# Kernel optimization log

Hardware: AMD Instinct MI355X
Metric: run time of the kernel (lower is better)

## Reference

```python
import jax, jax.numpy as jnp
import numpy as np

NB, NC = 100000, 10000   # buildings, communities
EB, EC = 400000, 80000   # edges
BD, CD = 64, 32          # feature dims


def _glorot(key, shape):
    fan_in = shape[-2] if len(shape) > 1 else shape[0]
    return jax.random.normal(key, shape, jnp.float32) * (1.0 / np.sqrt(fan_in))


def setup_inputs() -> dict:
    key = jax.random.key(0)
    ks = iter(jax.random.split(key, 40))
    inp = {}
    inp['building_features'] = jax.random.normal(next(ks), (NB, BD), jnp.float32)
    inp['community_features'] = jax.random.normal(next(ks), (NC, CD), jnp.float32)
    inp['building_edge_index'] = jax.random.randint(next(ks), (2, EB), 0, NB, jnp.int32)
    inp['community_edge_index'] = jax.random.randint(next(ks), (2, EC), 0, NC, jnp.int32)
    inp['building_to_comm_mapping'] = jax.random.randint(next(ks), (NB,), 0, NC, jnp.int32)
    inp['c1_wl'] = _glorot(next(ks), (CD, 512)); inp['c1_wr'] = _glorot(next(ks), (CD, 512))
    inp['c1_att'] = _glorot(next(ks), (8, 64)); inp['c1_b'] = jnp.zeros((512,), jnp.float32)
    inp['c2_wl'] = _glorot(next(ks), (512, 128)); inp['c2_wr'] = _glorot(next(ks), (512, 128))
    inp['c2_att'] = _glorot(next(ks), (4, 32)); inp['c2_b'] = jnp.zeros((128,), jnp.float32)
    # feature attention: 8 heads of MLP (64+128)->128->2
    inp['fa_w1'] = _glorot(next(ks), (8, BD + 128, 128)); inp['fa_b1'] = jnp.zeros((8, 128), jnp.float32)
    inp['fa_w2'] = _glorot(next(ks), (8, 128, 2)); inp['fa_b2'] = jnp.zeros((8, 2), jnp.float32)
    inp['b1_wl'] = _glorot(next(ks), (BD + 128, 512)); inp['b1_wr'] = _glorot(next(ks), (BD + 128, 512))
    inp['b1_att'] = _glorot(next(ks), (8, 64)); inp['b1_b'] = jnp.zeros((512,), jnp.float32)
    inp['b2_wl'] = _glorot(next(ks), (512, 128)); inp['b2_wr'] = _glorot(next(ks), (512, 128))
    inp['b2_att'] = _glorot(next(ks), (4, 32)); inp['b2_b'] = jnp.zeros((128,), jnp.float32)
    inp['b3_wl'] = _glorot(next(ks), (128, 2)); inp['b3_wr'] = _glorot(next(ks), (128, 2))
    inp['b3_att'] = _glorot(next(ks), (1, 2)); inp['b3_b'] = jnp.zeros((2,), jnp.float32)
    return inp


def gatv2(x, src, dst, wl, wr, att, b, heads, out_dim, concat=True):
    """PyG GATv2Conv (eval mode, self-loops already appended to src/dst)."""
    n = x.shape[0]
    xl = (x @ wl).reshape(n, heads, out_dim)  # source transform
    xr = (x @ wr).reshape(n, heads, out_dim)  # target transform
    e = jax.nn.leaky_relu(xl[src] + xr[dst], 0.2)          # [E,H,D]
    logits = jnp.einsum('ehd,hd->eh', e, att)              # [E,H]
    m = jax.ops.segment_max(logits, dst, num_segments=n)   # stable softmax per target
    p = jnp.exp(logits - m[dst])
    denom = jax.ops.segment_sum(p, dst, num_segments=n)
    alpha = p / denom[dst]
    agg = jax.ops.segment_sum(alpha[:, :, None] * xl[src], dst, num_segments=n)
    agg = agg.reshape(n, heads * out_dim) if concat else agg.mean(axis=1)
    return agg + b


def _with_self_loops(edge_index, n):
    loops = jnp.arange(n, dtype=edge_index.dtype)
    return (jnp.concatenate([edge_index[0], loops]), jnp.concatenate([edge_index[1], loops]))


def _forward(building_features, community_features,
             c1_wl, c1_wr, c1_att, c1_b, c2_wl, c2_wr, c2_att, c2_b,
             fa_w1, fa_b1, fa_w2, fa_b2,
             b1_wl, b1_wr, b1_att, b1_b, b2_wl, b2_wr, b2_att, b2_b,
             b3_wl, b3_wr, b3_att, b3_b,
             building_edge_index, community_edge_index, building_to_comm_mapping):
    csrc, cdst = _with_self_loops(community_edge_index, NC)
    bsrc, bdst = _with_self_loops(building_edge_index, NB)
    # community GNN (dropout is identity in eval)
    cx = jax.nn.relu(gatv2(community_features, csrc, cdst, c1_wl, c1_wr, c1_att, c1_b, 8, 64))
    cx = jax.nn.relu(gatv2(cx, csrc, cdst, c2_wl, c2_wr, c2_att, c2_b, 4, 32))  # [NC,128]
    bcf = cx[building_to_comm_mapping]                                          # [NB,128]
    # multi-head feature attention fusion (vectorized over 8 heads)
    combined = jnp.concatenate([building_features, bcf], axis=1)                # [NB,192]
    h = jax.nn.relu(jnp.einsum('nf,hfk->nhk', combined, fa_w1) + fa_b1)         # [NB,8,128]
    w = jax.nn.softmax(jnp.einsum('nhk,hko->nho', h, fa_w2) + fa_b2, axis=-1)   # [NB,8,2]
    wmean = w.mean(axis=1)                                                      # mean over heads == mean of weighted copies
    fused = jnp.concatenate([building_features * wmean[:, 0:1], bcf * wmean[:, 1:2]], axis=1)
    # building GNN (single batched graph == Batch.from_data_list over all communities)
    x = jax.nn.relu(gatv2(fused, bsrc, bdst, b1_wl, b1_wr, b1_att, b1_b, 8, 64))
    x = jax.nn.relu(gatv2(x, bsrc, bdst, b2_wl, b2_wr, b2_att, b2_b, 4, 32))
    x = gatv2(x, bsrc, bdst, b3_wl, b3_wr, b3_att, b3_b, 1, 2)                   # [NB,2]
    return jax.nn.log_softmax(x, axis=1)


def reference(building_features, community_features,
              c1_wl, c1_wr, c1_att, c1_b, c2_wl, c2_wr, c2_att, c2_b,
              fa_w1, fa_b1, fa_w2, fa_b2,
              b1_wl, b1_wr, b1_att, b1_b, b2_wl, b2_wr, b2_att, b2_b,
              b3_wl, b3_wr, b3_att, b3_b,
              building_edge_index, community_edge_index, building_to_comm_mapping):
    return _forward(building_features, community_features,
                    c1_wl, c1_wr, c1_att, c1_b, c2_wl, c2_wr, c2_att, c2_b,
                    fa_w1, fa_b1, fa_w2, fa_b2,
                    b1_wl, b1_wr, b1_att, b1_b, b2_wl, b2_wr, b2_att, b2_b,
                    b3_wl, b3_wr, b3_att, b3_b,
                    building_edge_index, community_edge_index, building_to_comm_mapping)
```

## Files before the change

kernel.cpp:

```cpp
#include <hip/hip_runtime.h>

static constexpr int NBLD = 100000, NCOM = 10000, EBU = 400000, ECO = 80000;
static constexpr int EBT = EBU + NBLD;
static constexpr int ECT = ECO + NCOM;

typedef _Float16 f16;
typedef _Float16 f16x2 __attribute__((ext_vector_type(2)));
typedef _Float16 f16x8 __attribute__((ext_vector_type(8)));
typedef float f32x4 __attribute__((ext_vector_type(4)));

static constexpr size_t OFF_X1H  = 0;
static constexpr size_t OFF_CXL  = 0;
static constexpr size_t OFF_CXR  = 10240000;
static constexpr size_t OFF_CX1  = 20480000;
static constexpr size_t OFF_CX2L = 30720000;
static constexpr size_t OFF_CX2R = 33280000;
static constexpr size_t OFF_X2   = 0;
static constexpr size_t OFF_XLH  = 102400000;
static constexpr size_t OFF_XRH  = 128000000;
static constexpr size_t OFF_XL2  = 102400000;
static constexpr size_t OFF_XR2  = 128000000;
static constexpr size_t OFF_BF16 = 153600000;
static constexpr size_t OFF_CXF16= 166400000;
static constexpr size_t OFF_WM   = 168960000;
static constexpr size_t OFF_XL3  = 169760000;
static constexpr size_t OFF_XR3  = 170560000;
static constexpr size_t OFF_FAW  = 171360000;
static constexpr size_t OFF_B1LT = 171753216;
static constexpr size_t OFF_B1RT = 171949824;
static constexpr size_t OFF_B2T  = 172146432;
static constexpr size_t OFF_BOFF = 172408576;
static constexpr size_t OFF_BCUR = 172808592;
static constexpr size_t OFF_BSRC = 173208592;
static constexpr size_t OFF_COFF = 175208592;
static constexpr size_t OFF_CCUR = 175248608;
static constexpr size_t OFF_CSRC = 175288608;
static constexpr size_t OFF_SC1  = 175648608;
static constexpr size_t OFF_SC2  = 175649632;
static constexpr size_t OFF_C1T  = 175700000;
static constexpr size_t OFF_C2T  = 175765536;
static constexpr size_t OFF_CF16 = 176027680;

__global__ void k_zero(int* __restrict__ p, int n) {
  int i = blockIdx.x * blockDim.x + threadIdx.x;
  if (i < n) p[i] = 0;
}

__global__ void k_zerof(float* __restrict__ p, int n) {
  int i = blockIdx.x * blockDim.x + threadIdx.x;
  if (i < n) p[i] = 0.f;
}

__global__ void k_cvt4(const float* __restrict__ a, f16* __restrict__ b, int n4) {
  int i = blockIdx.x * blockDim.x + threadIdx.x;
  if (i >= n4) return;
  float4 f = *(const float4*)(a + (size_t)i * 4);
  f16x2 h0; h0[0] = (f16)f.x; h0[1] = (f16)f.y;
  f16x2 h1; h1[0] = (f16)f.z; h1[1] = (f16)f.w;
  *(unsigned*)(b + (size_t)i * 4)     = __builtin_bit_cast(unsigned, h0);
  *(unsigned*)(b + (size_t)i * 4 + 2) = __builtin_bit_cast(unsigned, h1);
}

__global__ void k_cvtwb(const float* __restrict__ W, f16* __restrict__ WT, int K, int N) {
  int i = blockIdx.x * blockDim.x + threadIdx.x;
  if (i >= K * N) return;
  const float* Wb = W + (size_t)blockIdx.y * K * N;
  f16* Tb = WT + (size_t)blockIdx.y * K * N;
  int n = i / K, k = i - n * K;
  Tb[(size_t)n * K + k] = (f16)Wb[(size_t)k * N + n];
}

__global__ void k_count(const int* __restrict__ dsti, int Eg, int Et, int* __restrict__ cnt) {
  int e = blockIdx.x * blockDim.x + threadIdx.x;
  if (e >= Et) return;
  int dst = (e < Eg) ? dsti[e] : (e - Eg);
  atomicAdd(&cnt[dst], 1);
}

__global__ void k_scan1(const int* __restrict__ cnt, int N, int* __restrict__ off, int* __restrict__ bsum) {
  __shared__ int sh[256];
  int tid = threadIdx.x;
  int base = blockIdx.x * 2048 + tid * 8;
  int c[8]; int s = 0;
#pragma unroll
  for (int j = 0; j < 8; ++j) { int i = base + j; c[j] = (i < N) ? cnt[i] : 0; s += c[j]; }
  sh[tid] = s; __syncthreads();
  int own = s;
  for (int o = 1; o < 256; o <<= 1) {
    int v = (tid >= o) ? sh[tid - o] : 0; __syncthreads();
    sh[tid] += v; __syncthreads();
  }
  int ex = sh[tid] - own;
#pragma unroll
  for (int j = 0; j < 8; ++j) { int i = base + j; if (i < N) off[i] = ex; ex += c[j]; }
  if (tid == 255) bsum[blockIdx.x] = sh[255];
}

__global__ void k_scan2(const int* __restrict__ bsum, int nb, int* __restrict__ bpre) {
  __shared__ int sh[256];
  int tid = threadIdx.x;
  int v0 = (tid < nb) ? bsum[tid] : 0;
  sh[tid] = v0; __syncthreads();
  for (int o = 1; o < 256; o <<= 1) {
    int v = (tid >= o) ? sh[tid - o] : 0; __syncthreads();
    sh[tid] += v; __syncthreads();
  }
  bpre[tid] = sh[tid] - v0;
}

__global__ void k_scan3(int* __restrict__ off, int N, const int* __restrict__ bpre, int Et) {
  int i = blockIdx.x * blockDim.x + threadIdx.x;
  if (i < N) off[i] += bpre[i >> 11];
  if (i == 0) off[N] = Et;
}

__global__ void k_copycur(const int* __restrict__ off, int* __restrict__ cur, int N) {
  int i = blockIdx.x * blockDim.x + threadIdx.x;
  if (i < N) cur[i] = off[i];
}

__global__ void k_scatter(const int* __restrict__ srci, const int* __restrict__ dsti, int Eg, int Et,
                          int* __restrict__ cur, int* __restrict__ srcl) {
  int e = blockIdx.x * blockDim.x + threadIdx.x;
  if (e >= Et) return;
  int src, dst;
  if (e < Eg) { src = srci[e]; dst = dsti[e]; } else { src = dst = e - Eg; }
  int pos = atomicAdd(&cur[dst], 1);
  srcl[pos] = src;
}


static __device__ inline void stage_BT(f16 (*Bs)[40], const f16* __restrict__ WT, int ldk,
                                       int k0, int tid) {
  int col = tid >> 1, half = tid & 1;
  const f16* p = WT + (size_t)col * ldk + k0 + half * 16;
  *(uint4*)&Bs[col][half * 16]     = *(const uint4*)(p);
  *(uint4*)&Bs[col][half * 16 + 8] = *(const uint4*)(p + 8);
}

static __device__ inline void stage_BTpair(f16 (*Bs)[40], const f16* __restrict__ WLt,
                                           const f16* __restrict__ WRt, int ldk, int slab,
                                           int k0, int tid) {
  int col = tid >> 1, half = tid & 1;
  const f16* base = (col < 64) ? (WLt + (size_t)(slab + col) * ldk)
                               : (WRt + (size_t)(slab + col - 64) * ldk);
  const f16* p = base + k0 + half * 16;
  *(uint4*)&Bs[col][half * 16]     = *(const uint4*)(p);
  *(uint4*)&Bs[col][half * 16 + 8] = *(const uint4*)(p + 8);
}

template<bool SCALE>
static __device__ inline void stage_A16(f16 (*As)[40], const f16* __restrict__ bf16h,
                                        const f16* __restrict__ cx16, int mrow,
                                        f16 s0, f16 s1, int k0, int tid, int grow, int M) {
  int row = tid >> 1, half = tid & 1;
  int gc = k0 + half * 16;
  f16x8 v0 = {}, v1 = {};
  if (grow < M) {
    const f16* src; f16 s;
    if (gc < 64) { src = bf16h + (size_t)grow * 64 + gc; s = s0; }
    else         { src = cx16 + (size_t)mrow * 128 + (gc - 64); s = s1; }
    v0 = *(const f16x8*)(src);
    v1 = *(const f16x8*)(src + 8);
    if (SCALE) {
#pragma unroll
      for (int j = 0; j < 8; ++j) { v0[j] *= s; v1[j] *= s; }
    }
  }
  *(f16x8*)&As[row][half * 16]     = v0;
  *(f16x8*)&As[row][half * 16 + 8] = v1;
}

static __device__ inline void stage_Ah(f16 (*As)[40], const f16* __restrict__ Xh, int lda,
                                       int k0, int tid, int bm, int M) {
  int row = tid >> 1;
  int half = tid & 1;
  int grow = bm + row;
  uint4 u0 = make_uint4(0, 0, 0, 0), u1 = make_uint4(0, 0, 0, 0);
  if (grow < M) {
    const f16* p = Xh + (size_t)grow * lda + k0 + half * 16;
    u0 = *(const uint4*)(p);
    u1 = *(const uint4*)(p + 8);
  }
  *(uint4*)&As[row][half * 16]     = u0;
  *(uint4*)&As[row][half * 16 + 8] = u1;
}

static __device__ inline void mma_tiles(const f16 (*As)[40], const f16 (*Bs)[40],
                                        f32x4 acc[4][4], int wm, int wn, int lane) {
  int rl = lane & 15;
  int kg = (lane >> 4) * 8;
  f16x8 a[4], b[4];
#pragma unroll
  for (int i = 0; i < 4; ++i) a[i] = *(const f16x8*)&As[wm * 64 + i * 16 + rl][kg];
#pragma unroll
  for (int j = 0; j < 4; ++j) b[j] = *(const f16x8*)&Bs[wn * 64 + j * 16 + rl][kg];
#pragma unroll
  for (int i = 0; i < 4; ++i)
#pragma unroll
    for (int j = 0; j < 4; ++j)
      acc[i][j] = __builtin_amdgcn_mfma_f32_16x16x32_f16(a[i], b[j], acc[i][j], 0, 0, 0);
}

template<int NCB>
__global__ __launch_bounds__(256) void k_mgemm_gen(
    const f16* __restrict__ A, int lda,
    const f16* __restrict__ WT, int K,
    f16* __restrict__ out0, f16* __restrict__ out1, int N0, int ldo, int M) {
  __shared__ f16 As[128][40];
  __shared__ f16 Bs[128][40];
  int tid = threadIdx.x;
  int ppx = gridDim.x / (8 * NCB);
  int xcd = blockIdx.x & 7;
  int j6 = blockIdx.x >> 3;
  int cb = j6 % NCB;
  int p = xcd * ppx + j6 / NCB;
  int bm = p * 128;
  if (bm >= M) return;
  int bn = cb * 128;
  int lane = tid & 63, w = tid >> 6, wm_ = w >> 1, wn = w & 1;
  f32x4 acc[4][4];
#pragma unroll
  for (int i = 0; i < 4; ++i)
#pragma unroll
    for (int j = 0; j < 4; ++j) acc[i][j] = (f32x4){0.f, 0.f, 0.f, 0.f};

  const f16* WTb = WT + (size_t)bn * K;
  for (int k0 = 0; k0 < K; k0 += 32) {
    stage_Ah(As, A, lda, k0, tid, bm, M);
    stage_BT(Bs, WTb, K, k0, tid);
    __syncthreads();
    mma_tiles(As, Bs, acc, wm_, wn, lane);
    __syncthreads();
  }
  int rbase = bm + wm_ * 64 + (lane >> 4) * 4;
  int cl = lane & 15;
#pragma unroll
  for (int mi = 0; mi < 4; ++mi)
#pragma unroll
    for (int ni = 0; ni < 4; ++ni) {
      int col = bn + wn * 64 + ni * 16 + cl;
      f16* o; int c;
      if (col < N0) { o = out0; c = col; } else { o = out1; c = col - N0; }
#pragma unroll
      for (int r = 0; r < 4; ++r) {
        int row = rbase + mi * 16 + r;
        if (row < M) o[(size_t)row * ldo + c] = (f16)acc[mi][ni][r];
      }
    }
}

__global__ __launch_bounds__(256) void k_mgemm_b1(
    const f16* __restrict__ bf16h, const f16* __restrict__ cx16,
    const int* __restrict__ map, const float* __restrict__ wmv,
    const f16* __restrict__ WLt, const f16* __restrict__ WRt, int slabBase,
    f16* __restrict__ outl, f16* __restrict__ outr, int M) {
  __shared__ f16 As[128][40];
  __shared__ f16 Bs[128][40];
  int tid = threadIdx.x;
  int ppx = gridDim.x >> 4;
  int xcd = blockIdx.x & 7;
  int j6 = blockIdx.x >> 3;
  int ch = j6 & 1;
  int p = xcd * ppx + (j6 >> 1);
  int bm = p * 128;
  if (bm >= M) return;
  int slab = slabBase + ch * 64;
  int colbase = ch * 64;
  int lane = tid & 63, w = tid >> 6, wm_ = w >> 1, wn = w & 1;
  f32x4 acc[4][4];
#pragma unroll
  for (int i = 0; i < 4; ++i)
#pragma unroll
    for (int j = 0; j < 4; ++j) acc[i][j] = (f32x4){0.f, 0.f, 0.f, 0.f};

  int arow = bm + (tid >> 1);
  int mrow = 0; f16 s0 = (f16)1.f, s1 = (f16)1.f;
  if (arow < M) {
    mrow = map[arow];
    s0 = (f16)wmv[(size_t)arow * 2];
    s1 = (f16)wmv[(size_t)arow * 2 + 1];
  }

  for (int k0 = 0; k0 < 192; k0 += 32) {
    stage_A16<true>(As, bf16h, cx16, mrow, s0, s1, k0, tid, arow, M);
    stage_BTpair(Bs, WLt, WRt, 192, slab, k0, tid);
    __syncthreads();
    mma_tiles(As, Bs, acc, wm_, wn, lane);
    __syncthreads();
  }
  int rbase = bm + wm_ * 64 + (lane >> 4) * 4;
  int cl = lane & 15;
#pragma unroll
  for (int mi = 0; mi < 4; ++mi)
#pragma unroll
    for (int ni = 0; ni < 4; ++ni) {
      int col = wn * 64 + ni * 16 + cl;
      f16* o = (col < 64) ? outl : outr;
      int c = colbase + (col & 63);
#pragma unroll
      for (int r = 0; r < 4; ++r) {
        int row = rbase + mi * 16 + r;
        if (row < M) o[(size_t)row * 128 + c] = (f16)acc[mi][ni][r];
      }
    }
}

__global__ __launch_bounds__(256) void k_mgemm_fa(
    const f16* __restrict__ bf16h, const f16* __restrict__ cx16,
    const int* __restrict__ map,
    const f16* __restrict__ w1T, const float* __restrict__ b1,
    const float* __restrict__ w2, const float* __restrict__ b2,
    float* __restrict__ wmout, int M) {
  __shared__ f16 As[128][40];
  __shared__ f16 Bs[128][40];
  __shared__ float sred[128][4];
  int tid = threadIdx.x;
  int ppx = gridDim.x >> 6;
  int xcd = blockIdx.x & 7;
  int j6 = blockIdx.x >> 3;
  int p = xcd * ppx + (j6 >> 3);
  int h = j6 & 7;
  int bm = p * 128;
  if (bm >= M) return;
  int lane = tid & 63, w = tid >> 6, wm_ = w >> 1, wn = w & 1;
  f32x4 acc[4][4];
#pragma unroll
  for (int i = 0; i < 4; ++i)
#pragma unroll
    for (int j = 0; j < 4; ++j) acc[i][j] = (f32x4){0.f, 0.f, 0.f, 0.f};

  int arow = bm + (tid >> 1);
  int mrow = (arow < M) ? map[arow] : 0;
  const f16* WT = w1T + (size_t)h * 128 * 192;

  for (int k0 = 0; k0 < 192; k0 += 32) {
    stage_A16<false>(As, bf16h, cx16, mrow, (f16)1.f, (f16)1.f, k0, tid, arow, M);
    stage_BT(Bs, WT, 192, k0, tid);
    __syncthreads();
    mma_tiles(As, Bs, acc, wm_, wn, lane);
    __syncthreads();
  }

  int cl = lane & 15;
#pragma unroll
  for (int mi = 0; mi < 4; ++mi) {
    float t0[4] = {0.f, 0.f, 0.f, 0.f}, t1[4] = {0.f, 0.f, 0.f, 0.f};
#pragma unroll
    for (int ni = 0; ni < 4; ++ni) {
      int col = wn * 64 + ni * 16 + cl;
      float b1c = b1[h * 128 + col];
      float w0c = w2[((size_t)h * 128 + col) * 2];
      float w1c = w2[((size_t)h * 128 + col) * 2 + 1];
#pragma unroll
      for (int r = 0; r < 4; ++r) {
        float hv = fmaxf(acc[mi][ni][r] + b1c, 0.f);
        t0[r] = fmaf(hv, w0c, t0[r]);
        t1[r] = fmaf(hv, w1c, t1[r]);
      }
    }
#pragma unroll
    for (int m = 1; m < 16; m <<= 1) {
#pragma unroll
      for (int r = 0; r < 4; ++r) { t0[r] += __shfl_xor(t0[r], m); t1[r] += __shfl_xor(t1[r], m); }
    }
    if (cl == 0) {
#pragma unroll
      for (int r = 0; r < 4; ++r) {
        int rib = wm_ * 64 + mi * 16 + (lane >> 4) * 4 + r;
        sred[rib][wn] = t0[r];
        sred[rib][2 + wn] = t1[r];
      }
    }
  }
  __syncthreads();
  if (tid < 128) {
    int grow = bm + tid;
    if (grow < M) {
      float l0 = sred[tid][0] + sred[tid][1] + b2[h * 2];
      float l1 = sred[tid][2] + sred[tid][3] + b2[h * 2 + 1];
      float mx = fmaxf(l0, l1);
      float e0 = __expf(l0 - mx), e1 = __expf(l1 - mx);
      float inv = 0.125f / (e0 + e1);
      atomicAdd(&wmout[(size_t)grow * 2], e0 * inv);
      atomicAdd(&wmout[(size_t)grow * 2 + 1], e1 * inv);
    }
  }
}

template<int V, int G, bool RELU, typename IT, typename OT>
__global__ __launch_bounds__(256) void k_convf(const IT* __restrict__ xl, const IT* __restrict__ xr,
                                               const float* __restrict__ attw, const float* __restrict__ bias,
                                               const int* __restrict__ off, const int* __restrict__ srcl,
                                               OT* __restrict__ outp, int N, int ldx, int ldo) {
  int n = (int)((blockIdx.x * (unsigned)blockDim.x + threadIdx.x) >> 6);
  if (n >= N) return;
  int lane = threadIdx.x & 63;
  int base = lane * V;
  float xr_r[V], att_r[V], acc[V];
#pragma unroll
  for (int j = 0; j < V; ++j) {
    xr_r[j] = (float)xr[(size_t)n * ldx + base + j];
    att_r[j] = attw[base + j];
    acc[j] = 0.f;
  }
  float mh = -INFINITY, lh = 0.f;
  int p0 = off[n], p1 = off[n + 1];
  for (int p = p0; p < p1; ++p) {
    int src = srcl[p];
    float xlv[V];
    if constexpr (V == 2 && sizeof(IT) == 2) {
      f16x2 t = *(const f16x2*)(&xl[(size_t)src * ldx + base]);
      xlv[0] = (float)t[0]; xlv[1] = (float)t[1];
    } else if constexpr (V == 8 && sizeof(IT) == 2) {
      f16x8 t = *(const f16x8*)(&xl[(size_t)src * ldx + base]);
#pragma unroll
      for (int j = 0; j < 8; ++j) xlv[j] = (float)t[j];
    } else {
#pragma unroll
      for (int j = 0; j < V; ++j) xlv[j] = (float)xl[(size_t)src * ldx + base + j];
    }
    float part = 0.f;
#pragma unroll
    for (int j = 0; j < V; ++j) {
      float t = xlv[j] + xr_r[j];
      t = t > 0.f ? t : 0.2f * t;
      part = fmaf(t, att_r[j], part);
    }
#pragma unroll
    for (int m = 1; m < G; m <<= 1) part += __shfl_xor(part, m);
    float mn = fmaxf(mh, part);
    float scl = __expf(mh - mn);
    float pe = __expf(part - mn);
    lh = lh * scl + pe;
#pragma unroll
    for (int j = 0; j < V; ++j) acc[j] = acc[j] * scl + pe * xlv[j];
    mh = mn;
  }
  float inv = 1.f / lh;
#pragma unroll
  for (int j = 0; j < V; ++j) {
    float v = fmaf(acc[j], inv, bias[base + j]);
    if (RELU) v = fmaxf(v, 0.f);
    outp[(size_t)n * ldo + base + j] = (OT)v;
  }
}

__global__ __launch_bounds__(256) void k_b3gemm(const float* __restrict__ x2, const float* __restrict__ wl,
                                                const float* __restrict__ wr,
                                                float* __restrict__ xl3, float* __restrict__ xr3, int NB) {
  int n = (int)((blockIdx.x * (unsigned)blockDim.x + threadIdx.x) >> 6);
  if (n >= NB) return;
  int lane = threadIdx.x & 63;
  float2 a = *(const float2*)(x2 + (size_t)n * 128 + lane * 2);
  float4 wlv = *(const float4*)(wl + lane * 4);
  float4 wrv = *(const float4*)(wr + lane * 4);
  float l0 = a.x * wlv.x + a.y * wlv.z;
  float l1 = a.x * wlv.y + a.y * wlv.w;
  float r0 = a.x * wrv.x + a.y * wrv.z;
  float r1 = a.x * wrv.y + a.y * wrv.w;
#pragma unroll
  for (int m = 1; m < 64; m <<= 1) {
    l0 += __shfl_xor(l0, m); l1 += __shfl_xor(l1, m);
    r0 += __shfl_xor(r0, m); r1 += __shfl_xor(r1, m);
  }
  if (lane == 0) {
    xl3[(size_t)n * 2] = l0; xl3[(size_t)n * 2 + 1] = l1;
    xr3[(size_t)n * 2] = r0; xr3[(size_t)n * 2 + 1] = r1;
  }
}

__global__ void k_conv3(const float* __restrict__ xl, const float* __restrict__ xr,
                        const float* __restrict__ att, const float* __restrict__ bias,
                        const int* __restrict__ off, const int* __restrict__ srcl,
                        float* __restrict__ out, int NB) {
  int n = blockIdx.x * blockDim.x + threadIdx.x;
  if (n >= NB) return;
  float a0 = att[0], a1 = att[1];
  float xr0 = xr[(size_t)n * 2], xr1 = xr[(size_t)n * 2 + 1];
  float mh = -INFINITY, lh = 0.f, c0 = 0.f, c1 = 0.f;
  int p0 = off[n], p1 = off[n + 1];
  for (int p = p0; p < p1; ++p) {
    int src = srcl[p];
    float sl0 = xl[(size_t)src * 2], sl1 = xl[(size_t)src * 2 + 1];
    float t0 = sl0 + xr0; t0 = t0 > 0.f ? t0 : 0.2f * t0;
    float t1 = sl1 + xr1; t1 = t1 > 0.f ? t1 : 0.2f * t1;
    float lg = t0 * a0 + t1 * a1;
    float mn = fmaxf(mh, lg);
    float scl = __expf(mh - mn);
    float pe = __expf(lg - mn);
    lh = lh * scl + pe;
    c0 = c0 * scl + pe * sl0;
    c1 = c1 * scl + pe * sl1;
    mh = mn;
  }
  float inv = 1.f / lh;
  float v0 = c0 * inv + bias[0];
  float v1 = c1 * inv + bias[1];
  float mx = fmaxf(v0, v1);
  float ls = mx + logf(__expf(v0 - mx) + __expf(v1 - mx));
  out[(size_t)n * 2] = v0 - ls;
  out[(size_t)n * 2 + 1] = v1 - ls;
}

static inline int cdiv(int a, int b) { return (a + b - 1) / b; }

extern "C" void kernel_launch(void* const* d_in, const int* in_sizes, int n_in,
                              void* d_out, int out_size, void* d_ws, size_t ws_size,
                              hipStream_t stream) {
  (void)in_sizes; (void)n_in; (void)out_size; (void)ws_size;
  const float* bfeat = (const float*)d_in[0];
  const float* cfeat = (const float*)d_in[1];
  const int* bei = (const int*)d_in[2];
  const int* cei = (const int*)d_in[3];
  const int* b2c = (const int*)d_in[4];
  const float* c1_wl = (const float*)d_in[5];
  const float* c1_wr = (const float*)d_in[6];
  const float* c1_att = (const float*)d_in[7];
  const float* c1_b = (const float*)d_in[8];
  const float* c2_wl = (const float*)d_in[9];
  const float* c2_wr = (const float*)d_in[10];
  const float* c2_att = (const float*)d_in[11];
  const float* c2_b = (const float*)d_in[12];
  const float* fa_w1 = (const float*)d_in[13];
  const float* fa_b1 = (const float*)d_in[14];
  const float* fa_w2 = (const float*)d_in[15];
  const float* fa_b2 = (const float*)d_in[16];
  const float* b1_wl = (const float*)d_in[17];
  const float* b1_wr = (const float*)d_in[18];
  const float* b1_att = (const float*)d_in[19];
  const float* b1_b = (const float*)d_in[20];
  const float* b2_wl = (const float*)d_in[21];
  const float* b2_wr = (const float*)d_in[22];
  const float* b2_att = (const float*)d_in[23];
  const float* b2_b = (const float*)d_in[24];
  const float* b3_wl = (const float*)d_in[25];
  const float* b3_wr = (const float*)d_in[26];
  const float* b3_att = (const float*)d_in[27];
  const float* b3_b = (const float*)d_in[28];
  char* ws = (char*)d_ws;
  float* out = (float*)d_out;

  const int* b_src_arr = bei;
  const int* b_dst_arr = bei + EBU;
  const int* c_src_arr = cei;
  const int* c_dst_arr = cei + ECO;

  f16*   X1H  = (f16*)(ws + OFF_X1H);
  float* X2   = (float*)(ws + OFF_X2);
  f16*   XLH  = (f16*)(ws + OFF_XLH);
  f16*   XRH  = (f16*)(ws + OFF_XRH);
  f16*   XL2  = (f16*)(ws + OFF_XL2);
  f16*   XR2  = (f16*)(ws + OFF_XR2);
  f16*   CXLh = (f16*)(ws + OFF_CXL);
  f16*   CXRh = (f16*)(ws + OFF_CXR);
  f16*   CX1h = (f16*)(ws + OFF_CX1);
  f16*   CX2Lh= (f16*)(ws + OFF_CX2L);
  f16*   CX2Rh= (f16*)(ws + OFF_CX2R);
  f16*   BF16 = (f16*)(ws + OFF_BF16);
  f16*   CXF16= (f16*)(ws + OFF_CXF16);
  float* WM   = (float*)(ws + OFF_WM);
  float* XL3  = (float*)(ws + OFF_XL3);
  float* XR3  = (float*)(ws + OFF_XR3);
  f16*   FAW  = (f16*)(ws + OFF_FAW);
  f16*   B1LT = (f16*)(ws + OFF_B1LT);
  f16*   B1RT = (f16*)(ws + OFF_B1RT);
  f16*   B2T  = (f16*)(ws + OFF_B2T);
  f16*   C1T  = (f16*)(ws + OFF_C1T);
  f16*   C2T  = (f16*)(ws + OFF_C2T);
  f16*   CF16 = (f16*)(ws + OFF_CF16);
  int* BOFF = (int*)(ws + OFF_BOFF);
  int* BCUR = (int*)(ws + OFF_BCUR);
  int* BSRC = (int*)(ws + OFF_BSRC);
  int* COFF = (int*)(ws + OFF_COFF);
  int* CCUR = (int*)(ws + OFF_CCUR);
  int* CSRC = (int*)(ws + OFF_CSRC);
  int* SC1  = (int*)(ws + OFF_SC1);
  int* SC2  = (int*)(ws + OFF_SC2);

  k_cvtwb<<<dim3(cdiv(192 * 128, 256), 8), 256, 0, stream>>>(fa_w1, FAW, 192, 128);
  k_cvtwb<<<dim3(cdiv(192 * 512, 256), 1), 256, 0, stream>>>(b1_wl, B1LT, 192, 512);
  k_cvtwb<<<dim3(cdiv(192 * 512, 256), 1), 256, 0, stream>>>(b1_wr, B1RT, 192, 512);
  k_cvtwb<<<dim3(cdiv(512 * 128, 256), 1), 256, 0, stream>>>(b2_wl, B2T, 512, 128);
  k_cvtwb<<<dim3(cdiv(512 * 128, 256), 1), 256, 0, stream>>>(b2_wr, B2T + 128 * 512, 512, 128);
  k_cvtwb<<<dim3(cdiv(32 * 512, 256), 1), 256, 0, stream>>>(c1_wl, C1T, 32, 512);
  k_cvtwb<<<dim3(cdiv(32 * 512, 256), 1), 256, 0, stream>>>(c1_wr, C1T + 512 * 32, 32, 512);
  k_cvtwb<<<dim3(cdiv(512 * 128, 256), 1), 256, 0, stream>>>(c2_wl, C2T, 512, 128);
  k_cvtwb<<<dim3(cdiv(512 * 128, 256), 1), 256, 0, stream>>>(c2_wr, C2T + 128 * 512, 512, 128);
  k_cvt4<<<cdiv(NBLD * 16, 256), 256, 0, stream>>>(bfeat, BF16, NBLD * 16);
  k_cvt4<<<cdiv(NCOM * 8, 256), 256, 0, stream>>>(cfeat, CF16, NCOM * 8);

  k_zero<<<cdiv(NBLD, 256), 256, 0, stream>>>(BCUR, NBLD);
  k_count<<<cdiv(EBT, 256), 256, 0, stream>>>(b_dst_arr, EBU, EBT, BCUR);
  k_scan1<<<cdiv(NBLD, 2048), 256, 0, stream>>>(BCUR, NBLD, BOFF, SC1);
  k_scan2<<<1, 256, 0, stream>>>(SC1, cdiv(NBLD, 2048), SC2);
  k_scan3<<<cdiv(NBLD, 256), 256, 0, stream>>>(BOFF, NBLD, SC2, EBT);
  k_copycur<<<cdiv(NBLD, 256), 256, 0, stream>>>(BOFF, BCUR, NBLD);
  k_scatter<<<cdiv(EBT, 256), 256, 0, stream>>>(b_src_arr, b_dst_arr, EBU, EBT, BCUR, BSRC);
  k_zero<<<cdiv(NCOM, 256), 256, 0, stream>>>(CCUR, NCOM);
  k_count<<<cdiv(ECT, 256), 256, 0, stream>>>(c_dst_arr, ECO, ECT, CCUR);
  k_scan1<<<cdiv(NCOM, 2048), 256, 0, stream>>>(CCUR, NCOM, COFF, SC1);
  k_scan2<<<1, 256, 0, stream>>>(SC1, cdiv(NCOM, 2048), SC2);
  k_scan3<<<cdiv(NCOM, 256), 256, 0, stream>>>(COFF, NCOM, SC2, ECT);
  k_copycur<<<cdiv(NCOM, 256), 256, 0, stream>>>(COFF, CCUR, NCOM);
  k_scatter<<<cdiv(ECT, 256), 256, 0, stream>>>(c_src_arr, c_dst_arr, ECO, ECT, CCUR, CSRC);

  {
    int pC = cdiv(cdiv(NCOM, 128), 8);
    k_mgemm_gen<8><<<8 * pC * 8, 256, 0, stream>>>(
        CF16, 32, C1T, 32, CXLh, CXRh, 512, 512, NCOM);
    k_convf<8, 8, true, f16, f16><<<cdiv(NCOM, 4), 256, 0, stream>>>(
        CXLh, CXRh, c1_att, c1_b, COFF, CSRC, CX1h, NCOM, 512, 512);
    k_mgemm_gen<2><<<8 * pC * 2, 256, 0, stream>>>(
        CX1h, 512, C2T, 512, CX2Lh, CX2Rh, 128, 128, NCOM);
    k_convf<2, 16, true, f16, f16><<<cdiv(NCOM, 4), 256, 0, stream>>>(
        CX2Lh, CX2Rh, c2_att, c2_b, COFF, CSRC, CXF16, NCOM, 128, 128);
  }

  k_zerof<<<cdiv(NBLD * 2, 256), 256, 0, stream>>>(WM, NBLD * 2);
  {
    int panels = cdiv(NBLD, 128);
    int ppx = cdiv(panels, 8);
    k_mgemm_fa<<<64 * ppx, 256, 0, stream>>>(
        BF16, CXF16, b2c, FAW, fa_b1, fa_w2, fa_b2, WM, NBLD);
  }

  {
    int pB = cdiv(cdiv(NBLD, 128), 8);
    for (int cp = 0; cp < 4; ++cp) {
      k_mgemm_b1<<<16 * pB, 256, 0, stream>>>(
          BF16, CXF16, b2c, WM, B1LT, B1RT, cp * 128, XLH, XRH, NBLD);
      k_convf<2, 32, true, f16, f16><<<cdiv(NBLD, 4), 256, 0, stream>>>(
          XLH, XRH, b1_att + cp * 128, b1_b + cp * 128, BOFF, BSRC, X1H + cp * 128, NBLD, 128, 512);
    }
    k_mgemm_gen<2><<<8 * pB * 2, 256, 0, stream>>>(
        X1H, 512, B2T, 512, XL2, XR2, 128, 128, NBLD);
  }

  k_convf<2, 16, true, f16, float><<<cdiv(NBLD, 4), 256, 0, stream>>>(
      XL2, XR2, b2_att, b2_b, BOFF, BSRC, X2, NBLD, 128, 128);

  k_b3gemm<<<cdiv(NBLD, 4), 256, 0, stream>>>(X2, b3_wl, b3_wr, XL3, XR3, NBLD);
  k_conv3<<<cdiv(NBLD, 256), 256, 0, stream>>>(XL3, XR3, b3_att, b3_b, BOFF, BSRC, out, NBLD);
}
```

Baseline: 979.6 us.

## Merge preprocessing launches and double-buffer GEMM K-tiles through registers

Nine weight-transpose launches are folded into one 2D-grid kernel. The building and community CSR construction (zero, count, scan, copy, scatter) is merged into joint kernels, and the offset-to-cursor copy is folded into the scan fixup. The three GEMM kernels now prefetch the next two K-slices into registers while computing on double-buffered shared memory tiles. This cuts launch count and barrier frequency, at the cost of twice the shared memory per block and higher register pressure.

```diff
diff --git a/kernel.cpp b/kernel.cpp
--- a/kernel.cpp
+++ b/kernel.cpp
@@ -37,14 +37,11 @@
 static constexpr size_t OFF_CSRC = 175288608;
 static constexpr size_t OFF_SC1  = 175648608;
 static constexpr size_t OFF_SC2  = 175649632;
+static constexpr size_t OFF_SC1C = 175650656;
+static constexpr size_t OFF_SC2C = 175651680;
 static constexpr size_t OFF_C1T  = 175700000;
 static constexpr size_t OFF_C2T  = 175765536;
 static constexpr size_t OFF_CF16 = 176027680;
-
-__global__ void k_zero(int* __restrict__ p, int n) {
-  int i = blockIdx.x * blockDim.x + threadIdx.x;
-  if (i < n) p[i] = 0;
-}
 
 __global__ void k_zerof(float* __restrict__ p, int n) {
   int i = blockIdx.x * blockDim.x + threadIdx.x;
@@ -61,23 +58,57 @@
   *(unsigned*)(b + (size_t)i * 4 + 2) = __builtin_bit_cast(unsigned, h1);
 }
 
-__global__ void k_cvtwb(const float* __restrict__ W, f16* __restrict__ WT, int K, int N) {
+__global__ void k_cvtall(const float* __restrict__ fa_w1,
+                         const float* __restrict__ b1_wl, const float* __restrict__ b1_wr,
+                         const float* __restrict__ b2_wl, const float* __restrict__ b2_wr,
+                         const float* __restrict__ c1_wl, const float* __restrict__ c1_wr,
+                         const float* __restrict__ c2_wl, const float* __restrict__ c2_wr,
+                         f16* __restrict__ FAW, f16* __restrict__ B1LT, f16* __restrict__ B1RT,
+                         f16* __restrict__ B2T, f16* __restrict__ C1T, f16* __restrict__ C2T) {
+  int seg = blockIdx.y;
+  const float* W; f16* T; int K, N;
+  if (seg < 8)        { W = fa_w1 + (size_t)seg * 192 * 128; T = FAW + (size_t)seg * 128 * 192; K = 192; N = 128; }
+  else if (seg == 8)  { W = b1_wl; T = B1LT; K = 192; N = 512; }
+  else if (seg == 9)  { W = b1_wr; T = B1RT; K = 192; N = 512; }
+  else if (seg == 10) { W = b2_wl; T = B2T;  K = 512; N = 128; }
+  else if (seg == 11) { W = b2_wr; T = B2T + 128 * 512; K = 512; N = 128; }
+  else if (seg == 12) { W = c1_wl; T = C1T;  K = 32;  N = 512; }
+  else if (seg == 13) { W = c1_wr; T = C1T + 512 * 32; K = 32; N = 512; }
+  else if (seg == 14) { W = c2_wl; T = C2T;  K = 512; N = 128; }
+  else                { W = c2_wr; T = C2T + 128 * 512; K = 512; N = 128; }
   int i = blockIdx.x * blockDim.x + threadIdx.x;
   if (i >= K * N) return;
-  const float* Wb = W + (size_t)blockIdx.y * K * N;
-  f16* Tb = WT + (size_t)blockIdx.y * K * N;
   int n = i / K, k = i - n * K;
-  Tb[(size_t)n * K + k] = (f16)Wb[(size_t)k * N + n];
-}
-
-__global__ void k_count(const int* __restrict__ dsti, int Eg, int Et, int* __restrict__ cnt) {
+  T[(size_t)n * K + k] = (f16)W[(size_t)k * N + n];
+}
+
+__global__ void k_zero2(int* __restrict__ a, int na, int* __restrict__ b, int nb) {
+  int i = blockIdx.x * blockDim.x + threadIdx.x;
+  if (i < na) a[i] = 0;
+  else if (i - na < nb) b[i - na] = 0;
+}
+
+__global__ void k_count2(const int* __restrict__ bdst, const int* __restrict__ cdst,
+                         int* __restrict__ bcnt, int* __restrict__ ccnt) {
   int e = blockIdx.x * blockDim.x + threadIdx.x;
-  if (e >= Et) return;
-  int dst = (e < Eg) ? dsti[e] : (e - Eg);
-  atomicAdd(&cnt[dst], 1);
-}
-
-__global__ void k_scan1(const int* __restrict__ cnt, int N, int* __restrict__ off, int* __restrict__ bsum) {
+  if (e < EBT) {
+    int dst = (e < EBU) ? bdst[e] : (e - EBU);
+    atomicAdd(&bcnt[dst], 1);
+  } else {
+    int e2 = e - EBT;
+    if (e2 >= ECT) return;
+    int dst = (e2 < ECO) ? cdst[e2] : (e2 - ECO);
+    atomicAdd(&ccnt[dst], 1);
+  }
+}
+
+__global__ void k_scan1g(const int* __restrict__ bcnt, const int* __restrict__ ccnt,
+                         int* __restrict__ boff, int* __restrict__ coff,
+                         int* __restrict__ bsum, int* __restrict__ csum) {
+  const int* cnt = blockIdx.y ? ccnt : bcnt;
+  int* off = blockIdx.y ? coff : boff;
+  int* sum = blockIdx.y ? csum : bsum;
+  int N = blockIdx.y ? NCOM : NBLD;
   __shared__ int sh[256];
   int tid = threadIdx.x;
   int base = blockIdx.x * 2048 + tid * 8;
@@ -93,97 +124,116 @@
   int ex = sh[tid] - own;
 #pragma unroll
   for (int j = 0; j < 8; ++j) { int i = base + j; if (i < N) off[i] = ex; ex += c[j]; }
-  if (tid == 255) bsum[blockIdx.x] = sh[255];
-}
-
-__global__ void k_scan2(const int* __restrict__ bsum, int nb, int* __restrict__ bpre) {
+  if (tid == 255) sum[blockIdx.x] = sh[255];
+}
+
+__global__ void k_scan2g(const int* __restrict__ bsum, const int* __restrict__ csum,
+                         int nb, int nc, int* __restrict__ bpre, int* __restrict__ cpre) {
+  const int* sum = blockIdx.x ? csum : bsum;
+  int n = blockIdx.x ? nc : nb;
+  int* pre = blockIdx.x ? cpre : bpre;
   __shared__ int sh[256];
   int tid = threadIdx.x;
-  int v0 = (tid < nb) ? bsum[tid] : 0;
+  int v0 = (tid < n) ? sum[tid] : 0;
   sh[tid] = v0; __syncthreads();
   for (int o = 1; o < 256; o <<= 1) {
     int v = (tid >= o) ? sh[tid - o] : 0; __syncthreads();
     sh[tid] += v; __syncthreads();
   }
-  bpre[tid] = sh[tid] - v0;
-}
-
-__global__ void k_scan3(int* __restrict__ off, int N, const int* __restrict__ bpre, int Et) {
+  pre[tid] = sh[tid] - v0;
+}
+
+__global__ void k_scan3c(int* __restrict__ off, int N, const int* __restrict__ bpre, int Et,
+                         int* __restrict__ cur) {
   int i = blockIdx.x * blockDim.x + threadIdx.x;
-  if (i < N) off[i] += bpre[i >> 11];
+  if (i < N) {
+    int v = off[i] + bpre[i >> 11];
+    off[i] = v;
+    cur[i] = v;
+  }
   if (i == 0) off[N] = Et;
 }
 
-__global__ void k_copycur(const int* __restrict__ off, int* __restrict__ cur, int N) {
-  int i = blockIdx.x * blockDim.x + threadIdx.x;
-  if (i < N) cur[i] = off[i];
-}
-
-__global__ void k_scatter(const int* __restrict__ srci, const int* __restrict__ dsti, int Eg, int Et,
-                          int* __restrict__ cur, int* __restrict__ srcl) {
+__global__ void k_scatter2(const int* __restrict__ bsrc, const int* __restrict__ bdst,
+                           const int* __restrict__ csrc, const int* __restrict__ cdst,
+                           int* __restrict__ bcur, int* __restrict__ ccur,
+                           int* __restrict__ bout, int* __restrict__ cout) {
   int e = blockIdx.x * blockDim.x + threadIdx.x;
-  if (e >= Et) return;
-  int src, dst;
-  if (e < Eg) { src = srci[e]; dst = dsti[e]; } else { src = dst = e - Eg; }
-  int pos = atomicAdd(&cur[dst], 1);
-  srcl[pos] = src;
-}
-
-
-static __device__ inline void stage_BT(f16 (*Bs)[40], const f16* __restrict__ WT, int ldk,
-                                       int k0, int tid) {
+  if (e < EBT) {
+    int s, d;
+    if (e < EBU) { s = bsrc[e]; d = bdst[e]; } else { s = d = e - EBU; }
+    bout[atomicAdd(&bcur[d], 1)] = s;
+  } else {
+    int e2 = e - EBT;
+    if (e2 >= ECT) return;
+    int s, d;
+    if (e2 < ECO) { s = csrc[e2]; d = cdst[e2]; } else { s = d = e2 - ECO; }
+    cout[atomicAdd(&ccur[d], 1)] = s;
+  }
+}
+
+
+struct frag32 { f16x8 v0, v1; };
+
+static __device__ inline frag32 loadA_lin(const f16* __restrict__ X, int lda,
+                                          int k0, int tid, int bm, int M) {
+  int row = tid >> 1, half = tid & 1;
+  int grow = bm + row;
+  frag32 r; r.v0 = (f16x8){}; r.v1 = (f16x8){};
+  if (grow < M) {
+    const f16* p = X + (size_t)grow * lda + k0 + half * 16;
+    r.v0 = *(const f16x8*)(p);
+    r.v1 = *(const f16x8*)(p + 8);
+  }
+  return r;
+}
+
+template<bool SCALE>
+static __device__ inline frag32 loadA_fused(const f16* __restrict__ bf16h,
+                                            const f16* __restrict__ cx16, int mrow,
+                                            f16 s0, f16 s1, int k0, int tid, int grow, int M) {
+  int half = tid & 1;
+  int gc = k0 + half * 16;
+  frag32 r; r.v0 = (f16x8){}; r.v1 = (f16x8){};
+  if (grow < M) {
+    const f16* src; f16 s;
+    if (gc < 64) { src = bf16h + (size_t)grow * 64 + gc; s = s0; }
+    else         { src = cx16 + (size_t)mrow * 128 + (gc - 64); s = s1; }
+    r.v0 = *(const f16x8*)(src);
+    r.v1 = *(const f16x8*)(src + 8);
+    if (SCALE) {
+#pragma unroll
+      for (int j = 0; j < 8; ++j) { r.v0[j] *= s; r.v1[j] *= s; }
+    }
+  }
+  return r;
+}
+
+static __device__ inline frag32 loadB_T(const f16* __restrict__ WT, int ldk, int k0, int tid) {
   int col = tid >> 1, half = tid & 1;
   const f16* p = WT + (size_t)col * ldk + k0 + half * 16;
-  *(uint4*)&Bs[col][half * 16]     = *(const uint4*)(p);
-  *(uint4*)&Bs[col][half * 16 + 8] = *(const uint4*)(p + 8);
-}
-
-static __device__ inline void stage_BTpair(f16 (*Bs)[40], const f16* __restrict__ WLt,
-                                           const f16* __restrict__ WRt, int ldk, int slab,
-                                           int k0, int tid) {
+  frag32 r;
+  r.v0 = *(const f16x8*)(p);
+  r.v1 = *(const f16x8*)(p + 8);
+  return r;
+}
+
+static __device__ inline frag32 loadB_Tpair(const f16* __restrict__ WLt, const f16* __restrict__ WRt,
+                                            int ldk, int slab, int k0, int tid) {
   int col = tid >> 1, half = tid & 1;
   const f16* base = (col < 64) ? (WLt + (size_t)(slab + col) * ldk)
                                : (WRt + (size_t)(slab + col - 64) * ldk);
   const f16* p = base + k0 + half * 16;
-  *(uint4*)&Bs[col][half * 16]     = *(const uint4*)(p);
-  *(uint4*)&Bs[col][half * 16 + 8] = *(const uint4*)(p + 8);
-}
-
-template<bool SCALE>
-static __device__ inline void stage_A16(f16 (*As)[40], const f16* __restrict__ bf16h,
-                                        const f16* __restrict__ cx16, int mrow,
-                                        f16 s0, f16 s1, int k0, int tid, int grow, int M) {
+  frag32 r;
+  r.v0 = *(const f16x8*)(p);
+  r.v1 = *(const f16x8*)(p + 8);
+  return r;
+}
+
+static __device__ inline void writeFrag(f16 (*S)[40], frag32 f, int tid) {
   int row = tid >> 1, half = tid & 1;
-  int gc = k0 + half * 16;
-  f16x8 v0 = {}, v1 = {};
-  if (grow < M) {
-    const f16* src; f16 s;
-    if (gc < 64) { src = bf16h + (size_t)grow * 64 + gc; s = s0; }
-    else         { src = cx16 + (size_t)mrow * 128 + (gc - 64); s = s1; }
-    v0 = *(const f16x8*)(src);
-    v1 = *(const f16x8*)(src + 8);
-    if (SCALE) {
-#pragma unroll
-      for (int j = 0; j < 8; ++j) { v0[j] *= s; v1[j] *= s; }
-    }
-  }
-  *(f16x8*)&As[row][half * 16]     = v0;
-  *(f16x8*)&As[row][half * 16 + 8] = v1;
-}
-
-static __device__ inline void stage_Ah(f16 (*As)[40], const f16* __restrict__ Xh, int lda,
-                                       int k0, int tid, int bm, int M) {
-  int row = tid >> 1;
-  int half = tid & 1;
-  int grow = bm + row;
-  uint4 u0 = make_uint4(0, 0, 0, 0), u1 = make_uint4(0, 0, 0, 0);
-  if (grow < M) {
-    const f16* p = Xh + (size_t)grow * lda + k0 + half * 16;
-    u0 = *(const uint4*)(p);
-    u1 = *(const uint4*)(p + 8);
-  }
-  *(uint4*)&As[row][half * 16]     = u0;
-  *(uint4*)&As[row][half * 16 + 8] = u1;
+  *(f16x8*)&S[row][half * 16]     = f.v0;
+  *(f16x8*)&S[row][half * 16 + 8] = f.v1;
 }
 
 static __device__ inline void mma_tiles(const f16 (*As)[40], const f16 (*Bs)[40],
@@ -207,8 +257,8 @@
     const f16* __restrict__ A, int lda,
     const f16* __restrict__ WT, int K,
     f16* __restrict__ out0, f16* __restrict__ out1, int N0, int ldo, int M) {
-  __shared__ f16 As[128][40];
-  __shared__ f16 Bs[128][40];
+  __shared__ f16 As[2][128][40];
+  __shared__ f16 Bs[2][128][40];
   int tid = threadIdx.x;
   int ppx = gridDim.x / (8 * NCB);
   int xcd = blockIdx.x & 7;
@@ -226,11 +276,27 @@
     for (int j = 0; j < 4; ++j) acc[i][j] = (f32x4){0.f, 0.f, 0.f, 0.f};
 
   const f16* WTb = WT + (size_t)bn * K;
-  for (int k0 = 0; k0 < K; k0 += 32) {
-    stage_Ah(As, A, lda, k0, tid, bm, M);
-    stage_BT(Bs, WTb, K, k0, tid);
+  int NT = K >> 5;
+  frag32 a0 = loadA_lin(A, lda, 0, tid, bm, M);
+  frag32 b0 = loadB_T(WTb, K, 0, tid);
+  frag32 a1; a1.v0 = (f16x8){}; a1.v1 = (f16x8){};
+  frag32 b1v = a1;
+  if (NT > 1) { a1 = loadA_lin(A, lda, 32, tid, bm, M); b1v = loadB_T(WTb, K, 32, tid); }
+  for (int t = 0; t < NT; t += 2) {
+    writeFrag(As[0], a0, tid); writeFrag(Bs[0], b0, tid);
+    bool two = (t + 1 < NT);
+    if (two) { writeFrag(As[1], a1, tid); writeFrag(Bs[1], b1v, tid); }
     __syncthreads();
-    mma_tiles(As, Bs, acc, wm_, wn, lane);
+    if (t + 2 < NT) {
+      a0 = loadA_lin(A, lda, (t + 2) * 32, tid, bm, M);
+      b0 = loadB_T(WTb, K, (t + 2) * 32, tid);
+      if (t + 3 < NT) {
+        a1 = loadA_lin(A, lda, (t + 3) * 32, tid, bm, M);
+        b1v = loadB_T(WTb, K, (t + 3) * 32, tid);
+      }
+    }
+    mma_tiles(As[0], Bs[0], acc, wm_, wn, lane);
+    if (two) mma_tiles(As[1], Bs[1], acc, wm_, wn, lane);
     __syncthreads();
   }
   int rbase = bm + wm_ * 64 + (lane >> 4) * 4;
@@ -255,8 +321,8 @@
     const int* __restrict__ map, const float* __restrict__ wmv,
     const f16* __restrict__ WLt, const f16* __restrict__ WRt, int slabBase,
     f16* __restrict__ outl, f16* __restrict__ outr, int M) {
-  __shared__ f16 As[128][40];
-  __shared__ f16 Bs[128][40];
+  __shared__ f16 As[2][128][40];
+  __shared__ f16 Bs[2][128][40];
   int tid = threadIdx.x;
   int ppx = gridDim.x >> 4;
   int xcd = blockIdx.x & 7;
@@ -282,11 +348,22 @@
     s1 = (f16)wmv[(size_t)arow * 2 + 1];
   }
 
-  for (int k0 = 0; k0 < 192; k0 += 32) {
-    stage_A16<true>(As, bf16h, cx16, mrow, s0, s1, k0, tid, arow, M);
-    stage_BTpair(Bs, WLt, WRt, 192, slab, k0, tid);
+  frag32 a0 = loadA_fused<true>(bf16h, cx16, mrow, s0, s1, 0, tid, arow, M);
+  frag32 b0 = loadB_Tpair(WLt, WRt, 192, slab, 0, tid);
+  frag32 a1 = loadA_fused<true>(bf16h, cx16, mrow, s0, s1, 32, tid, arow, M);
+  frag32 b1v = loadB_Tpair(WLt, WRt, 192, slab, 32, tid);
+  for (int t = 0; t < 6; t += 2) {
+    writeFrag(As[0], a0, tid); writeFrag(Bs[0], b0, tid);
+    writeFrag(As[1], a1, tid); writeFrag(Bs[1], b1v, tid);
     __syncthreads();
-    mma_tiles(As, Bs, acc, wm_, wn, lane);
+    if (t + 2 < 6) {
+      a0 = loadA_fused<true>(bf16h, cx16, mrow, s0, s1, (t + 2) * 32, tid, arow, M);
+      b0 = loadB_Tpair(WLt, WRt, 192, slab, (t + 2) * 32, tid);
+      a1 = loadA_fused<true>(bf16h, cx16, mrow, s0, s1, (t + 3) * 32, tid, arow, M);
+      b1v = loadB_Tpair(WLt, WRt, 192, slab, (t + 3) * 32, tid);
+    }
+    mma_tiles(As[0], Bs[0], acc, wm_, wn, lane);
+    mma_tiles(As[1], Bs[1], acc, wm_, wn, lane);
     __syncthreads();
   }
   int rbase = bm + wm_ * 64 + (lane >> 4) * 4;
@@ -312,8 +389,8 @@
     const f16* __restrict__ w1T, const float* __restrict__ b1,
     const float* __restrict__ w2, const float* __restrict__ b2,
     float* __restrict__ wmout, int M) {
-  __shared__ f16 As[128][40];
-  __shared__ f16 Bs[128][40];
+  __shared__ f16 As[2][128][40];
+  __shared__ f16 Bs[2][128][40];
   __shared__ float sred[128][4];
   int tid = threadIdx.x;
   int ppx = gridDim.x >> 6;
@@ -334,11 +411,22 @@
   int mrow = (arow < M) ? map[arow] : 0;
   const f16* WT = w1T + (size_t)h * 128 * 192;
 
-  for (int k0 = 0; k0 < 192; k0 += 32) {
-    stage_A16<false>(As, bf16h, cx16, mrow, (f16)1.f, (f16)1.f, k0, tid, arow, M);
-    stage_BT(Bs, WT, 192, k0, tid);
+  frag32 a0 = loadA_fused<false>(bf16h, cx16, mrow, (f16)1.f, (f16)1.f, 0, tid, arow, M);
+  frag32 b0 = loadB_T(WT, 192, 0, tid);
+  frag32 a1 = loadA_fused<false>(bf16h, cx16, mrow, (f16)1.f, (f16)1.f, 32, tid, arow, M);
+  frag32 b1v = loadB_T(WT, 192, 32, tid);
+  for (int t = 0; t < 6; t += 2) {
+    writeFrag(As[0], a0, tid); writeFrag(Bs[0], b0, tid);
+    writeFrag(As[1], a1, tid); writeFrag(Bs[1], b1v, tid);
     __syncthreads();
-    mma_tiles(As, Bs, acc, wm_, wn, lane);
+    if (t + 2 < 6) {
+      a0 = loadA_fused<false>(bf16h, cx16, mrow, (f16)1.f, (f16)1.f, (t + 2) * 32, tid, arow, M);
+      b0 = loadB_T(WT, 192, (t + 2) * 32, tid);
+      a1 = loadA_fused<false>(bf16h, cx16, mrow, (f16)1.f, (f16)1.f, (t + 3) * 32, tid, arow, M);
+      b1v = loadB_T(WT, 192, (t + 3) * 32, tid);
+    }
+    mma_tiles(As[0], Bs[0], acc, wm_, wn, lane);
+    mma_tiles(As[1], Bs[1], acc, wm_, wn, lane);
     __syncthreads();
   }
 
@@ -577,33 +665,23 @@
   int* CSRC = (int*)(ws + OFF_CSRC);
   int* SC1  = (int*)(ws + OFF_SC1);
   int* SC2  = (int*)(ws + OFF_SC2);
-
-  k_cvtwb<<<dim3(cdiv(192 * 128, 256), 8), 256, 0, stream>>>(fa_w1, FAW, 192, 128);
-  k_cvtwb<<<dim3(cdiv(192 * 512, 256), 1), 256, 0, stream>>>(b1_wl, B1LT, 192, 512);
-  k_cvtwb<<<dim3(cdiv(192 * 512, 256), 1), 256, 0, stream>>>(b1_wr, B1RT, 192, 512);
-  k_cvtwb<<<dim3(cdiv(512 * 128, 256), 1), 256, 0, stream>>>(b2_wl, B2T, 512, 128);
-  k_cvtwb<<<dim3(cdiv(512 * 128, 256), 1), 256, 0, stream>>>(b2_wr, B2T + 128 * 512, 512, 128);
-  k_cvtwb<<<dim3(cdiv(32 * 512, 256), 1), 256, 0, stream>>>(c1_wl, C1T, 32, 512);
-  k_cvtwb<<<dim3(cdiv(32 * 512, 256), 1), 256, 0, stream>>>(c1_wr, C1T + 512 * 32, 32, 512);
-  k_cvtwb<<<dim3(cdiv(512 * 128, 256), 1), 256, 0, stream>>>(c2_wl, C2T, 512, 128);
-  k_cvtwb<<<dim3(cdiv(512 * 128, 256), 1), 256, 0, stream>>>(c2_wr, C2T + 128 * 512, 512, 128);
+  int* SC1C = (int*)(ws + OFF_SC1C);
+  int* SC2C = (int*)(ws + OFF_SC2C);
+
+  k_cvtall<<<dim3(cdiv(192 * 512, 256), 16), 256, 0, stream>>>(
+      fa_w1, b1_wl, b1_wr, b2_wl, b2_wr, c1_wl, c1_wr, c2_wl, c2_wr,
+      FAW, B1LT, B1RT, B2T, C1T, C2T);
   k_cvt4<<<cdiv(NBLD * 16, 256), 256, 0, stream>>>(bfeat, BF16, NBLD * 16);
   k_cvt4<<<cdiv(NCOM * 8, 256), 256, 0, stream>>>(cfeat, CF16, NCOM * 8);
 
-  k_zero<<<cdiv(NBLD, 256), 256, 0, stream>>>(BCUR, NBLD);
-  k_count<<<cdiv(EBT, 256), 256, 0, stream>>>(b_dst_arr, EBU, EBT, BCUR);
-  k_scan1<<<cdiv(NBLD, 2048), 256, 0, stream>>>(BCUR, NBLD, BOFF, SC1);
-  k_scan2<<<1, 256, 0, stream>>>(SC1, cdiv(NBLD, 2048), SC2);
-  k_scan3<<<cdiv(NBLD, 256), 256, 0, stream>>>(BOFF, NBLD, SC2, EBT);
-  k_copycur<<<cdiv(NBLD, 256), 256, 0, stream>>>(BOFF, BCUR, NBLD);
-  k_scatter<<<cdiv(EBT, 256), 256, 0, stream>>>(b_src_arr, b_dst_arr, EBU, EBT, BCUR, BSRC);
-  k_zero<<<cdiv(NCOM, 256), 256, 0, stream>>>(CCUR, NCOM);
-  k_count<<<cdiv(ECT, 256), 256, 0, stream>>>(c_dst_arr, ECO, ECT, CCUR);
-  k_scan1<<<cdiv(NCOM, 2048), 256, 0, stream>>>(CCUR, NCOM, COFF, SC1);
-  k_scan2<<<1, 256, 0, stream>>>(SC1, cdiv(NCOM, 2048), SC2);
-  k_scan3<<<cdiv(NCOM, 256), 256, 0, stream>>>(COFF, NCOM, SC2, ECT);
-  k_copycur<<<cdiv(NCOM, 256), 256, 0, stream>>>(COFF, CCUR, NCOM);
-  k_scatter<<<cdiv(ECT, 256), 256, 0, stream>>>(c_src_arr, c_dst_arr, ECO, ECT, CCUR, CSRC);
+  k_zero2<<<cdiv(NBLD + NCOM, 256), 256, 0, stream>>>(BCUR, NBLD, CCUR, NCOM);
+  k_count2<<<cdiv(EBT + ECT, 256), 256, 0, stream>>>(b_dst_arr, c_dst_arr, BCUR, CCUR);
+  k_scan1g<<<dim3(cdiv(NBLD, 2048), 2), 256, 0, stream>>>(BCUR, CCUR, BOFF, COFF, SC1, SC1C);
+  k_scan2g<<<2, 256, 0, stream>>>(SC1, SC1C, cdiv(NBLD, 2048), cdiv(NCOM, 2048), SC2, SC2C);
+  k_scan3c<<<cdiv(NBLD, 256), 256, 0, stream>>>(BOFF, NBLD, SC2, EBT, BCUR);
+  k_scan3c<<<cdiv(NCOM, 256), 256, 0, stream>>>(COFF, NCOM, SC2C, ECT, CCUR);
+  k_scatter2<<<cdiv(EBT + ECT, 256), 256, 0, stream>>>(
+      b_src_arr, b_dst_arr, c_src_arr, c_dst_arr, BCUR, CCUR, BSRC, CSRC);
 
   {
     int pC = cdiv(cdiv(NCOM, 128), 8);
```

After: 942.4 us. 3.8% less time.
